# Kernel optimization log

Hardware: AMD Instinct MI355X
Metric: run time of the kernel (lower is better)

The kernel has to match this reference:

```python
import jax, jax.numpy as jnp
import numpy as np

EPS = 1e-5

def _leaky(x):
    return jax.nn.leaky_relu(x, 0.2)

def _bn(x, p, axis):
    # p: [4, C] rows = (gamma, beta, running_mean, running_var); inference-mode BN
    g, b, m, v = p
    scale = g * jax.lax.rsqrt(v + EPS)
    shape = [1] * x.ndim
    shape[axis] = -1
    return x * scale.reshape(shape) + (b - m * scale).reshape(shape)

def _graph_feature(x, k):
    # x: [B, C, N] -> edge features [B, 2C, N, k] (knn on -squared-distance, topk largest)
    B, C, N = x.shape
    xx = jnp.sum(x * x, axis=1)                                   # [B, N]
    pd = 2.0 * jnp.einsum('bcn,bcm->bnm', x, x) - xx[:, :, None] - xx[:, None, :]
    idx = jax.lax.top_k(pd, k)[1]                                 # [B, N, k]
    xt = jnp.transpose(x, (0, 2, 1))                              # [B, N, C]
    nb = xt[jnp.arange(B)[:, None, None], idx]                    # [B, N, k, C]
    ctr = xt[:, :, None, :]
    f = jnp.concatenate([nb - ctr, jnp.broadcast_to(ctr, nb.shape)], axis=-1)
    return jnp.transpose(f, (0, 3, 1, 2))                         # [B, 2C, N, k]

def _cbam(x, fc1, fc2, sw):
    # Channel attention (shared MLP on avg+max pooled) then spatial attention (5x5 conv)
    mlp = lambda v: jax.nn.relu(v @ fc1.T) @ fc2.T
    ca = jax.nn.sigmoid(mlp(jnp.mean(x, (2, 3))) + mlp(jnp.max(x, (2, 3))))
    x = x * ca[:, :, None, None]
    s = jnp.concatenate([jnp.mean(x, 1, keepdims=True), jnp.max(x, 1, keepdims=True)], axis=1)
    sa = jax.lax.conv_general_dilated(s, sw, (1, 1), [(2, 2), (2, 2)],
                                      dimension_numbers=('NCHW', 'OIHW', 'NCHW'))
    return x * jax.nn.sigmoid(sa)

def _edge_block(x, k, W, bn, fc1, fc2, sw):
    f = _graph_feature(x, k)                                      # [B, 2C, N, k]
    f = _leaky(_bn(jnp.einsum('oc,bcnk->bonk', W, f), bn, 1))     # 1x1 conv + BN + LeakyReLU
    f = _cbam(f, fc1, fc2, sw)
    return jnp.max(f, axis=-1)                                    # [B, Cout, N]

def _bn_params(key, c):
    k1, k2, k3, k4 = jax.random.split(key, 4)
    g = 1.0 + 0.1 * jax.random.normal(k1, (c,))
    b = 0.1 * jax.random.normal(k2, (c,))
    m = 0.1 * jax.random.normal(k3, (c,))
    v = 0.5 + jax.random.uniform(k4, (c,))
    return jnp.stack([g, b, m, v])

def setup_inputs() -> dict:
    key = jax.random.key(0)
    nrm = lambda i, shape, s: s * jax.random.normal(jax.random.fold_in(key, i), shape, dtype=jnp.float32)
    d = {}
    d['x'] = jax.random.normal(jax.random.fold_in(key, 0), (4, 3, 2048), dtype=jnp.float32)
    d['W1'] = nrm(1, (64, 6), 0.3)
    d['W2'] = nrm(2, (64, 128), 0.15)
    d['W3'] = nrm(3, (128, 128), 0.15)
    d['W4'] = nrm(4, (256, 256), 0.1)
    d['W5'] = nrm(5, (1024, 512), 0.08)
    for i, c in zip(range(1, 6), [64, 64, 128, 256, 1024]):
        d['bn%d' % i] = _bn_params(jax.random.fold_in(key, 10 + i), c)
    d['bn6'] = _bn_params(jax.random.fold_in(key, 16), 512)
    d['bn7'] = _bn_params(jax.random.fold_in(key, 17), 256)
    for j, c in zip(range(1, 5), [64, 64, 128, 256]):
        r = c // 8
        d['ca%d_fc1' % j] = nrm(20 + j, (r, c), 0.2)
        d['ca%d_fc2' % j] = nrm(30 + j, (c, r), 0.2)
        d['sa%d' % j] = nrm(40 + j, (1, 2, 5, 5), 0.2)
    d['lin1_w'] = nrm(50, (512, 2048), 0.05)
    d['lin2_w'] = nrm(51, (256, 512), 0.08)
    d['lin2_b'] = nrm(52, (256,), 0.05)
    d['lin3_w'] = nrm(53, (40, 256), 0.1)
    d['lin3_b'] = nrm(54, (40,), 0.05)
    d['k'] = 20
    return d

def reference(x, W1, bn1, ca1_fc1, ca1_fc2, sa1, W2, bn2, ca2_fc1, ca2_fc2, sa2,
              W3, bn3, ca3_fc1, ca3_fc2, sa3, W4, bn4, ca4_fc1, ca4_fc2, sa4,
              W5, bn5, lin1_w, bn6, lin2_w, lin2_b, bn7, lin3_w, lin3_b, k):
    x1 = _edge_block(x,  k, W1, bn1, ca1_fc1, ca1_fc2, sa1)   # [B, 64, N]
    x2 = _edge_block(x1, k, W2, bn2, ca2_fc1, ca2_fc2, sa2)   # [B, 64, N]
    x3 = _edge_block(x2, k, W3, bn3, ca3_fc1, ca3_fc2, sa3)   # [B, 128, N]
    x4 = _edge_block(x3, k, W4, bn4, ca4_fc1, ca4_fc2, sa4)   # [B, 256, N]
    xc = jnp.concatenate([x1, x2, x3, x4], axis=1)            # [B, 512, N]
    h = _leaky(_bn(jnp.einsum('oc,bcn->bon', W5, xc), bn5, 1))  # [B, 1024, N]
    g = jnp.concatenate([jnp.max(h, axis=-1), jnp.mean(h, axis=-1)], axis=1)  # [B, 2048]
    g = _leaky(_bn(g @ lin1_w.T, bn6, 1))                     # dropout = identity (eval)
    g = _leaky(_bn(g @ lin2_w.T + lin2_b, bn7, 1))
    return g @ lin3_w.T + lin3_b                              # [B, 40]
```

## Files before the change

kernel.cpp:

```cpp
#include <hip/hip_runtime.h>
#include <math.h>

#define BB 4
#define NN 2048
#define KK 20
#define EPSF 1e-5f
#define TR 4

__device__ __forceinline__ float leaky(float x){ return x > 0.f ? x : 0.2f*x; }
__device__ __forceinline__ float sigm(float x){ return 1.f/(1.f+expf(-x)); }

__global__ void k_xx(const float* __restrict__ X, long bstride, int C, float* __restrict__ xx){
  int i = blockIdx.x*blockDim.x + threadIdx.x;
  int b = i >> 11, n = i & (NN-1);
  const float* xb = X + (long)b*bstride;
  float s = 0.f;
  for (int c = 0; c < C; ++c){ float v = xb[c*NN + n]; s += v*v; }
  xx[i] = s;
}

__global__ __launch_bounds__(256) void k_knn(const float* __restrict__ X, long bstride, int C,
                      const float* __restrict__ xx, int* __restrict__ idx){
  __shared__ unsigned int pdrow[TR][NN];
  int rowsPerB = NN/TR;
  int b = blockIdx.x / rowsPerB;
  int r0 = (blockIdx.x % rowsPerB) * TR;
  const float* xb = X + (long)b*bstride;
  int tid = threadIdx.x;

  float acc[4][8];
  #pragma unroll
  for (int r = 0; r < 4; ++r)
    #pragma unroll
    for (int j = 0; j < 8; ++j) acc[r][j] = 0.f;
  for (int c = 0; c < C; ++c){
    const float* xcp = xb + (long)c*NN;
    float4 ctr = *(const float4*)(xcp + r0);
    float v[8];
    #pragma unroll
    for (int j = 0; j < 8; ++j) v[j] = xcp[tid + 256*j];
    #pragma unroll
    for (int j = 0; j < 8; ++j){
      acc[0][j] = fmaf(ctr.x, v[j], acc[0][j]);
      acc[1][j] = fmaf(ctr.y, v[j], acc[1][j]);
      acc[2][j] = fmaf(ctr.z, v[j], acc[2][j]);
      acc[3][j] = fmaf(ctr.w, v[j], acc[3][j]);
    }
  }
  float xxr[4];
  #pragma unroll
  for (int r = 0; r < 4; ++r) xxr[r] = xx[b*NN + r0 + r];
  #pragma unroll
  for (int j = 0; j < 8; ++j){
    int m = tid + 256*j;
    float xxm = xx[b*NN + m];
    #pragma unroll
    for (int r = 0; r < 4; ++r){
      float pd = 2.f*acc[r][j] - xxr[r] - xxm;
      unsigned u = __float_as_uint(pd);
      u ^= (u & 0x80000000u) ? 0xFFFFFFFFu : 0x80000000u;
      pdrow[r][m] = u;
    }
  }
  __syncthreads();

  int wave = tid >> 6, lane = tid & 63;
  int r = wave;
  unsigned long long k1 = 0ull, k2 = 0ull;
  #pragma unroll
  for (int j = 0; j < 32; ++j){
    int m = lane + (j<<6);
    unsigned long long key = ((unsigned long long)pdrow[r][m] << 11) | (unsigned)(2047 - m);
    if (key > k1){ k2 = k1; k1 = key; }
    else if (key > k2){ k2 = key; }
  }
  unsigned removed = 0u;
  int* orow = idx + ((long)b*NN + r0 + r)*KK;
  for (int sel = 0; sel < KK; ++sel){
    unsigned long long g = k1;
    #pragma unroll
    for (int off = 32; off; off >>= 1){
      unsigned long long o = __shfl_xor(g, off);
      if (o > g) g = o;
    }
    int gm = 2047 - (int)(g & 2047u);
    if (lane == 0) orow[sel] = gm;
    if ((gm & 63) == lane){
      removed |= 1u << (gm >> 6);
      k1 = k2; k2 = 0ull;
      if (k1 == 0ull){
        #pragma unroll
        for (int j = 0; j < 32; ++j){
          if (removed & (1u << j)) continue;
          int m = lane + (j<<6);
          unsigned long long key = ((unsigned long long)pdrow[r][m] << 11) | (unsigned)(2047 - m);
          if (key > k1){ k2 = k1; k1 = key; }
          else if (key > k2){ k2 = key; }
        }
      }
    }
  }
}

__global__ void k_proj(const float* __restrict__ X, long bstride, int C, int Cout,
                       const float* __restrict__ W, const float* __restrict__ bn,
                       float* __restrict__ Pg, float* __restrict__ PgT,
                       float* __restrict__ Pc, float* __restrict__ PcT){
  int nb = NN/256;
  int t = blockIdx.x;
  int nchunk = t % nb; t /= nb;
  int o = t % Cout; int b = t / Cout;
  int m = nchunk*256 + threadIdx.x;
  const float* xb = X + (long)b*bstride;
  float a1 = 0.f, a2 = 0.f;
  for (int c = 0; c < C; ++c){
    float v  = xb[c*NN + m];
    float wl = W[o*2*C + c], wr = W[o*2*C + C + c];
    a1 += wl*v; a2 += (wr - wl)*v;
  }
  float gg = bn[o], bb = bn[Cout+o], mn = bn[2*Cout+o], vv = bn[3*Cout+o];
  float scale = gg * rsqrtf(vv + EPSF);
  float bias  = bb - mn*scale;
  float pg = scale*a1;
  float pc = scale*a2 + bias;
  Pg [((long)b*Cout + o)*NN + m] = pg;
  PgT[((long)b*NN + m)*Cout + o] = pg;
  Pc [((long)b*Cout + o)*NN + m] = pc;
  PcT[((long)b*NN + m)*Cout + o] = pc;
}

__global__ __launch_bounds__(256) void k_proj_t(const float* __restrict__ X, long bstride, int C, int Cout,
                         const float* __restrict__ W, const float* __restrict__ bn,
                         float* __restrict__ Pg, float* __restrict__ PgT,
                         float* __restrict__ Pc, float* __restrict__ PcT){
  __shared__ float xs[32][128];
  __shared__ float wls[64][33];
  __shared__ float wds[64][33];
  int t = blockIdx.x;
  int nb = t & 15; t >>= 4;
  int nob = Cout >> 6;
  int ob = t % nob; int b = t / nob;
  int n0 = nb << 7, o0 = ob << 6;
  int tid = threadIdx.x;
  int tx = tid & 15, ty = tid >> 4;
  const float* xb = X + (long)b*bstride + n0;

  float ag[4][8], ac[4][8];
  #pragma unroll
  for (int i = 0; i < 4; ++i)
    #pragma unroll
    for (int j = 0; j < 8; ++j){ ag[i][j] = 0.f; ac[i][j] = 0.f; }

  for (int cc = 0; cc < C; cc += 32){
    {
      int col4 = tid & 31;
      int ci0 = tid >> 5;
      #pragma unroll
      for (int q = 0; q < 4; ++q){
        int ci = ci0 + (q << 3);
        float4 v = *(const float4*)(xb + (long)(cc + ci)*NN + (col4 << 2));
        *(float4*)&xs[ci][col4 << 2] = v;
      }
    }
    {
      int ci4 = tid & 7;
      int oi0 = tid >> 3;
      #pragma unroll
      for (int q = 0; q < 2; ++q){
        int oi = oi0 + (q << 5);
        const float* wrow = W + (long)(o0 + oi)*2*C + cc + (ci4 << 2);
        float4 wl = *(const float4*)(wrow);
        float4 wr = *(const float4*)(wrow + C);
        wls[oi][(ci4 << 2) + 0] = wl.x;
        wls[oi][(ci4 << 2) + 1] = wl.y;
        wls[oi][(ci4 << 2) + 2] = wl.z;
        wls[oi][(ci4 << 2) + 3] = wl.w;
        wds[oi][(ci4 << 2) + 0] = wr.x - wl.x;
        wds[oi][(ci4 << 2) + 1] = wr.y - wl.y;
        wds[oi][(ci4 << 2) + 2] = wr.z - wl.z;
        wds[oi][(ci4 << 2) + 3] = wr.w - wl.w;
      }
    }
    __syncthreads();
    #pragma unroll 8
    for (int ci = 0; ci < 32; ++ci){
      float4 xa  = *(const float4*)&xs[ci][tx << 2];
      float4 xc2 = *(const float4*)&xs[ci][64 + (tx << 2)];
      #pragma unroll
      for (int oo = 0; oo < 4; ++oo){
        float wl = wls[(ty << 2) + oo][ci];
        float wd = wds[(ty << 2) + oo][ci];
        ag[oo][0] = fmaf(wl, xa.x, ag[oo][0]); ag[oo][1] = fmaf(wl, xa.y, ag[oo][1]);
        ag[oo][2] = fmaf(wl, xa.z, ag[oo][2]); ag[oo][3] = fmaf(wl, xa.w, ag[oo][3]);
        ag[oo][4] = fmaf(wl, xc2.x, ag[oo][4]); ag[oo][5] = fmaf(wl, xc2.y, ag[oo][5]);
        ag[oo][6] = fmaf(wl, xc2.z, ag[oo][6]); ag[oo][7] = fmaf(wl, xc2.w, ag[oo][7]);
        ac[oo][0] = fmaf(wd, xa.x, ac[oo][0]); ac[oo][1] = fmaf(wd, xa.y, ac[oo][1]);
        ac[oo][2] = fmaf(wd, xa.z, ac[oo][2]); ac[oo][3] = fmaf(wd, xa.w, ac[oo][3]);
        ac[oo][4] = fmaf(wd, xc2.x, ac[oo][4]); ac[oo][5] = fmaf(wd, xc2.y, ac[oo][5]);
        ac[oo][6] = fmaf(wd, xc2.z, ac[oo][6]); ac[oo][7] = fmaf(wd, xc2.w, ac[oo][7]);
      }
    }
    __syncthreads();
  }

  float scl[4], bia[4];
  #pragma unroll
  for (int oo = 0; oo < 4; ++oo){
    int o = o0 + (ty << 2) + oo;
    scl[oo] = bn[o] * rsqrtf(bn[3*Cout + o] + EPSF);
    bia[oo] = bn[Cout + o] - bn[2*Cout + o]*scl[oo];
  }
  #pragma unroll
  for (int oo = 0; oo < 4; ++oo){
    long rb = ((long)b*Cout + o0 + (ty << 2) + oo)*NN + n0;
    float4 g0 = {scl[oo]*ag[oo][0], scl[oo]*ag[oo][1], scl[oo]*ag[oo][2], scl[oo]*ag[oo][3]};
    float4 g1 = {scl[oo]*ag[oo][4], scl[oo]*ag[oo][5], scl[oo]*ag[oo][6], scl[oo]*ag[oo][7]};
    float4 c0 = {fmaf(scl[oo], ac[oo][0], bia[oo]), fmaf(scl[oo], ac[oo][1], bia[oo]),
                 fmaf(scl[oo], ac[oo][2], bia[oo]), fmaf(scl[oo], ac[oo][3], bia[oo])};
    float4 c1 = {fmaf(scl[oo], ac[oo][4], bia[oo]), fmaf(scl[oo], ac[oo][5], bia[oo]),
                 fmaf(scl[oo], ac[oo][6], bia[oo]), fmaf(scl[oo], ac[oo][7], bia[oo])};
    *(float4*)(Pg + rb + (tx << 2))      = g0;
    *(float4*)(Pg + rb + 64 + (tx << 2)) = g1;
    *(float4*)(Pc + rb + (tx << 2))      = c0;
    *(float4*)(Pc + rb + 64 + (tx << 2)) = c1;
  }
  #pragma unroll
  for (int j = 0; j < 8; ++j){
    int n = n0 + ((j < 4) ? (tx << 2) + j : 64 + (tx << 2) + (j - 4));
    long rb = ((long)b*NN + n)*Cout + o0 + (ty << 2);
    float4 tg = {scl[0]*ag[0][j], scl[1]*ag[1][j], scl[2]*ag[2][j], scl[3]*ag[3][j]};
    float4 tc = {fmaf(scl[0], ac[0][j], bia[0]), fmaf(scl[1], ac[1][j], bia[1]),
                 fmaf(scl[2], ac[2][j], bia[2]), fmaf(scl[3], ac[3][j], bia[3])};
    *(float4*)(PgT + rb) = tg;
    *(float4*)(PcT + rb) = tc;
  }
}

__global__ void k_cstats(const float* __restrict__ Pg, const float* __restrict__ Pc,
                         const int* __restrict__ idx, int Cout,
                         float* __restrict__ cmean, float* __restrict__ cmax){
  int b = blockIdx.x / Cout, o = blockIdx.x % Cout;
  const float* pg = Pg + ((long)b*Cout + o)*NN;
  const float* pc = Pc + ((long)b*Cout + o)*NN;
  const int* id = idx + (long)b*NN*KK;
  int tid = threadIdx.x;
  float s = 0.f, mx = -INFINITY;
  for (int i = tid; i < NN*KK; i += 256){
    int n = i / KK;
    int iv = id[i];
    float v = leaky(pg[iv] + pc[n]);
    s += v; mx = fmaxf(mx, v);
  }
  __shared__ float ss[256], sm[256];
  ss[tid] = s; sm[tid] = mx; __syncthreads();
  for (int st = 128; st; st >>= 1){
    if (tid < st){ ss[tid] += ss[tid+st]; sm[tid] = fmaxf(sm[tid], sm[tid+st]); }
    __syncthreads();
  }
  if (tid == 0){ cmean[blockIdx.x] = ss[0]/(float)(NN*KK); cmax[blockIdx.x] = sm[0]; }
}

__global__ void k_catt(const float* __restrict__ cmean, const float* __restrict__ cmax,
                       const float* __restrict__ fc1, const float* __restrict__ fc2,
                       int Cout, int r, float* __restrict__ ca){
  int b = blockIdx.x, tid = threadIdx.x;
  __shared__ float h1m[32], h1x[32];
  __shared__ float mv[256], xv[256];
  if (tid < Cout){ mv[tid] = cmean[b*Cout+tid]; xv[tid] = cmax[b*Cout+tid]; }
  __syncthreads();
  if (tid < r){
    float am = 0.f, ax = 0.f;
    for (int c = 0; c < Cout; ++c){ float w = fc1[tid*Cout+c]; am += w*mv[c]; ax += w*xv[c]; }
    h1m[tid] = fmaxf(am, 0.f); h1x[tid] = fmaxf(ax, 0.f);
  }
  __syncthreads();
  if (tid < Cout){
    float a = 0.f;
    for (int j = 0; j < r; ++j) a += fc2[tid*r+j]*(h1m[j] + h1x[j]);
    ca[b*Cout+tid] = sigm(a);
  }
}

__global__ void k_sstats(const float* __restrict__ PgT, const float* __restrict__ PcT,
                         const int* __restrict__ idx, const float* __restrict__ ca,
                         int Cout, float* __restrict__ s){
  long i = (long)blockIdx.x*256 + threadIdx.x;
  int kk = (int)(i % KK); long t = i / KK; int n = (int)(t % NN); int b = (int)(t / NN);
  int iv = idx[((long)b*NN + n)*KK + kk];
  const float4* pg4 = (const float4*)(PgT + ((long)b*NN + iv)*Cout);
  const float4* pc4 = (const float4*)(PcT + ((long)b*NN + n)*Cout);
  const float4* ca4 = (const float4*)(ca + b*Cout);
  float sum = 0.f, mx = -INFINITY;
  int q = Cout >> 2;
  for (int o = 0; o < q; ++o){
    float4 a = pg4[o], c = pc4[o], w = ca4[o];
    float v0 = leaky(a.x + c.x) * w.x;
    float v1 = leaky(a.y + c.y) * w.y;
    float v2 = leaky(a.z + c.z) * w.z;
    float v3 = leaky(a.w + c.w) * w.w;
    sum += v0; mx = fmaxf(mx, v0);
    sum += v1; mx = fmaxf(mx, v1);
    sum += v2; mx = fmaxf(mx, v2);
    sum += v3; mx = fmaxf(mx, v3);
  }
  s[((long)b*2*NN + n)*KK + kk]      = sum/(float)Cout;
  s[((long)b*2*NN + NN + n)*KK + kk] = mx;
}

__global__ void k_sconv(const float* __restrict__ s, const float* __restrict__ sw,
                        float* __restrict__ sa){
  long i = (long)blockIdx.x*256 + threadIdx.x;
  int kk = (int)(i % KK); long t = i / KK; int n = (int)(t % NN); int b = (int)(t / NN);
  float acc = 0.f;
  for (int ci = 0; ci < 2; ++ci)
    for (int dy = 0; dy < 5; ++dy){
      int nn = n + dy - 2; if (nn < 0 || nn >= NN) continue;
      for (int dx = 0; dx < 5; ++dx){
        int kx = kk + dx - 2; if (kx < 0 || kx >= KK) continue;
        acc += sw[ci*25 + dy*5 + dx] * s[((long)b*2*NN + ci*NN + nn)*KK + kx];
      }
    }
  sa[i] = sigm(acc);
}

__global__ void k_final(const float* __restrict__ Pg, const float* __restrict__ Pc,
                        const int* __restrict__ idx, const float* __restrict__ ca,
                        const float* __restrict__ sa, int Cout, int outoff,
                        float* __restrict__ xc){
  long i = (long)blockIdx.x*256 + threadIdx.x;
  int n = (int)(i % NN); long t = i / NN; int o = (int)(t % Cout); int b = (int)(t / Cout);
  const float* pg = Pg + ((long)b*Cout + o)*NN;
  float pcv = Pc[((long)b*Cout + o)*NN + n];
  float cav = ca[b*Cout + o];
  const int* id   = idx + ((long)b*NN + n)*KK;
  const float* sb = sa  + ((long)b*NN + n)*KK;
  float mx = -INFINITY;
  for (int kk = 0; kk < KK; ++kk){
    float v = leaky(pg[id[kk]] + pcv) * cav * sb[kk];
    mx = fmaxf(mx, v);
  }
  xc[((long)b*512 + outoff + o)*NN + n] = mx;
}

__global__ __launch_bounds__(256) void k_gemm5(const float* __restrict__ xc, const float* __restrict__ W5,
                        const float* __restrict__ bn5, float* __restrict__ gpart){
  __shared__ float xs[32][128];
  __shared__ float wsd[64][33];
  int t = blockIdx.x;
  int nb = t & 15; t >>= 4;
  int ob = t & 15; int b = t >> 4;
  int n0 = nb << 7, o0 = ob << 6;
  int tid = threadIdx.x;
  int tx = tid & 15, ty = tid >> 4;
  const float* xb = xc + (long)b*512*NN + n0;

  float acc[4][8];
  #pragma unroll
  for (int i = 0; i < 4; ++i)
    #pragma unroll
    for (int j = 0; j < 8; ++j) acc[i][j] = 0.f;

  for (int cc = 0; cc < 16; ++cc){
    {
      int col4 = tid & 31;
      int ci0 = tid >> 5;
      #pragma unroll
      for (int q = 0; q < 4; ++q){
        int ci = ci0 + (q << 3);
        float4 v = *(const float4*)(xb + (long)(cc*32 + ci)*NN + (col4 << 2));
        *(float4*)&xs[ci][col4 << 2] = v;
      }
    }
    {
      int ci4 = tid & 7;
      int oi0 = tid >> 3;
      #pragma unroll
      for (int q = 0; q < 2; ++q){
        int oi = oi0 + (q << 5);
        float4 w = *(const float4*)(W5 + (long)(o0 + oi)*512 + cc*32 + (ci4 << 2));
        wsd[oi][(ci4 << 2) + 0] = w.x;
        wsd[oi][(ci4 << 2) + 1] = w.y;
        wsd[oi][(ci4 << 2) + 2] = w.z;
        wsd[oi][(ci4 << 2) + 3] = w.w;
      }
    }
    __syncthreads();
    #pragma unroll 8
    for (int ci = 0; ci < 32; ++ci){
      float4 xa = *(const float4*)&xs[ci][tx << 2];
      float4 xc2 = *(const float4*)&xs[ci][64 + (tx << 2)];
      float w0 = wsd[(ty << 2) + 0][ci];
      float w1 = wsd[(ty << 2) + 1][ci];
      float w2 = wsd[(ty << 2) + 2][ci];
      float w3 = wsd[(ty << 2) + 3][ci];
      acc[0][0] = fmaf(w0, xa.x, acc[0][0]); acc[0][1] = fmaf(w0, xa.y, acc[0][1]);
      acc[0][2] = fmaf(w0, xa.z, acc[0][2]); acc[0][3] = fmaf(w0, xa.w, acc[0][3]);
      acc[0][4] = fmaf(w0, xc2.x, acc[0][4]); acc[0][5] = fmaf(w0, xc2.y, acc[0][5]);
      acc[0][6] = fmaf(w0, xc2.z, acc[0][6]); acc[0][7] = fmaf(w0, xc2.w, acc[0][7]);
      acc[1][0] = fmaf(w1, xa.x, acc[1][0]); acc[1][1] = fmaf(w1, xa.y, acc[1][1]);
      acc[1][2] = fmaf(w1, xa.z, acc[1][2]); acc[1][3] = fmaf(w1, xa.w, acc[1][3]);
      acc[1][4] = fmaf(w1, xc2.x, acc[1][4]); acc[1][5] = fmaf(w1, xc2.y, acc[1][5]);
      acc[1][6] = fmaf(w1, xc2.z, acc[1][6]); acc[1][7] = fmaf(w1, xc2.w, acc[1][7]);
      acc[2][0] = fmaf(w2, xa.x, acc[2][0]); acc[2][1] = fmaf(w2, xa.y, acc[2][1]);
      acc[2][2] = fmaf(w2, xa.z, acc[2][2]); acc[2][3] = fmaf(w2, xa.w, acc[2][3]);
      acc[2][4] = fmaf(w2, xc2.x, acc[2][4]); acc[2][5] = fmaf(w2, xc2.y, acc[2][5]);
      acc[2][6] = fmaf(w2, xc2.z, acc[2][6]); acc[2][7] = fmaf(w2, xc2.w, acc[2][7]);
      acc[3][0] = fmaf(w3, xa.x, acc[3][0]); acc[3][1] = fmaf(w3, xa.y, acc[3][1]);
      acc[3][2] = fmaf(w3, xa.z, acc[3][2]); acc[3][3] = fmaf(w3, xa.w, acc[3][3]);
      acc[3][4] = fmaf(w3, xc2.x, acc[3][4]); acc[3][5] = fmaf(w3, xc2.y, acc[3][5]);
      acc[3][6] = fmaf(w3, xc2.z, acc[3][6]); acc[3][7] = fmaf(w3, xc2.w, acc[3][7]);
    }
    __syncthreads();
  }

  float psum[4], pmax[4];
  #pragma unroll
  for (int oo = 0; oo < 4; ++oo){
    int o = o0 + (ty << 2) + oo;
    float scale = bn5[o] * rsqrtf(bn5[3072 + o] + EPSF);
    float bias  = bn5[1024 + o] - bn5[2048 + o] * scale;
    float s = 0.f, mx = -INFINITY;
    #pragma unroll
    for (int j = 0; j < 8; ++j){
      float v = leaky(fmaf(scale, acc[oo][j], bias));
      s += v; mx = fmaxf(mx, v);
    }
    psum[oo] = s; pmax[oo] = mx;
  }
  __syncthreads();
  float* ps = &xs[0][0];
  float* pm = ps + 64*17;
  #pragma unroll
  for (int oo = 0; oo < 4; ++oo){
    int o = (ty << 2) + oo;
    ps[o*17 + tx] = psum[oo];
    pm[o*17 + tx] = pmax[oo];
  }
  __syncthreads();
  if (tid < 64){
    float s = 0.f, mx = -INFINITY;
    #pragma unroll
    for (int j = 0; j < 16; ++j){
      s += ps[tid*17 + j];
      mx = fmaxf(mx, pm[tid*17 + j]);
    }
    long base = ((long)(b*16 + nb))*1024 + o0 + tid;
    gpart[base] = s;
    gpart[65536 + base] = mx;
  }
}

__global__ void k_pool2(const float* __restrict__ gpart, float* __restrict__ g){
  int i = blockIdx.x*256 + threadIdx.x;
  int b = i >> 10, o = i & 1023;
  float s = 0.f, mx = -INFINITY;
  for (int nb = 0; nb < 16; ++nb){
    s += gpart[((long)(b*16 + nb))*1024 + o];
    mx = fmaxf(mx, gpart[65536 + ((long)(b*16 + nb))*1024 + o]);
  }
  g[b*2048 + o] = mx;
  g[b*2048 + 1024 + o] = s * (1.f/2048.f);
}

__global__ void k_dense(const float* __restrict__ in, const float* __restrict__ w,
                        const float* __restrict__ bias, const float* __restrict__ bnp,
                        int Cin, int Cout, float* __restrict__ out){
  int b = blockIdx.x / Cout, j = blockIdx.x % Cout;
  int tid = threadIdx.x;
  float a = 0.f;
  for (int c = tid; c < Cin; c += 256) a += w[(long)j*Cin + c]*in[(long)b*Cin + c];
  __shared__ float ss[256];
  ss[tid] = a; __syncthreads();
  for (int st = 128; st; st >>= 1){
    if (tid < st) ss[tid] += ss[tid+st];
    __syncthreads();
  }
  if (tid == 0){
    float v = ss[0];
    if (bias) v += bias[j];
    if (bnp){
      float scale = bnp[j]*rsqrtf(bnp[3*Cout+j] + EPSF);
      float bb    = bnp[Cout+j] - bnp[2*Cout+j]*scale;
      v = leaky(v*scale + bb);
    }
    out[b*Cout + j] = v;
  }
}

extern "C" void kernel_launch(void* const* d_in, const int* in_sizes, int n_in,
                              void* d_out, int out_size, void* d_ws, size_t ws_size,
                              hipStream_t stream){
  (void)in_sizes; (void)n_in; (void)out_size;
  const float* x  = (const float*)d_in[0];
  const float* Wb[4]  = {(const float*)d_in[1], (const float*)d_in[2], (const float*)d_in[3], (const float*)d_in[4]};
  const float* W5     = (const float*)d_in[5];
  const float* bnb[4] = {(const float*)d_in[6], (const float*)d_in[7], (const float*)d_in[8], (const float*)d_in[9]};
  const float* bn5    = (const float*)d_in[10];
  const float* bn6    = (const float*)d_in[11];
  const float* bn7    = (const float*)d_in[12];
  const float* fc1b[4] = {(const float*)d_in[13], (const float*)d_in[16], (const float*)d_in[19], (const float*)d_in[22]};
  const float* fc2b[4] = {(const float*)d_in[14], (const float*)d_in[17], (const float*)d_in[20], (const float*)d_in[23]};
  const float* swb[4]  = {(const float*)d_in[15], (const float*)d_in[18], (const float*)d_in[21], (const float*)d_in[24]};
  const float* lin1_w = (const float*)d_in[25];
  const float* lin2_w = (const float*)d_in[26];
  const float* lin2_b = (const float*)d_in[27];
  const float* lin3_w = (const float*)d_in[28];
  const float* lin3_b = (const float*)d_in[29];

  float* ws = (float*)d_ws;
  float* xc = ws;
  float* tb = ws + (size_t)BB*512*NN;
  float* xx   = tb;
  int*   idx  = (int*)(tb + 8192);
  float* Pg   = tb + 8192 + 163840;
  float* PgT  = Pg  + 2097152;
  float* Pc   = PgT + 2097152;
  float* PcT  = Pc  + 2097152;
  float* cmean = PcT + 2097152;
  float* cmax  = cmean + 1024;
  float* ca    = cmax + 1024;
  float* s     = ca + 1024;
  float* sa    = s + 327680;
  float* gpart = tb;
  float* g  = tb + 131072;
  float* t1 = g + 8192;
  float* t2 = t1 + 2048;
  size_t needed = ((size_t)BB*512*NN + 9055232) * 4;
  if (ws_size < needed) return;

  const int Cin [4] = {3, 64, 64, 128};
  const int Cout[4] = {64, 64, 128, 256};
  const int inoff[4]  = {0, 0, 64, 128};
  const int outoff[4] = {0, 64, 128, 256};

  for (int blk = 0; blk < 4; ++blk){
    const float* Xp; long bstr;
    if (blk == 0){ Xp = x; bstr = 3l*NN; }
    else { Xp = xc + (long)inoff[blk]*NN; bstr = 512l*NN; }
    int C = Cin[blk], Co = Cout[blk];
    hipLaunchKernelGGL(k_xx,    dim3(BB*NN/256), dim3(256), 0, stream, Xp, bstr, C, xx);
    hipLaunchKernelGGL(k_knn,   dim3(BB*NN/TR),  dim3(256), 0, stream, Xp, bstr, C, xx, idx);
    if (blk == 0){
      hipLaunchKernelGGL(k_proj,  dim3(BB*Co*(NN/256)), dim3(256), 0, stream, Xp, bstr, C, Co, Wb[blk], bnb[blk], Pg, PgT, Pc, PcT);
    } else {
      hipLaunchKernelGGL(k_proj_t, dim3(BB*(Co>>6)*16), dim3(256), 0, stream, Xp, bstr, C, Co, Wb[blk], bnb[blk], Pg, PgT, Pc, PcT);
    }
    hipLaunchKernelGGL(k_cstats, dim3(BB*Co), dim3(256), 0, stream, Pg, Pc, idx, Co, cmean, cmax);
    hipLaunchKernelGGL(k_catt,  dim3(BB), dim3(256), 0, stream, cmean, cmax, fc1b[blk], fc2b[blk], Co, Co/8, ca);
    hipLaunchKernelGGL(k_sstats, dim3(BB*NN*KK/256), dim3(256), 0, stream, PgT, PcT, idx, ca, Co, s);
    hipLaunchKernelGGL(k_sconv, dim3(BB*NN*KK/256), dim3(256), 0, stream, s, swb[blk], sa);
    hipLaunchKernelGGL(k_final, dim3(BB*Co*NN/256), dim3(256), 0, stream, Pg, Pc, idx, ca, sa, Co, outoff[blk], xc);
  }
  hipLaunchKernelGGL(k_gemm5, dim3(BB*16*16), dim3(256), 0, stream, xc, W5, bn5, gpart);
  hipLaunchKernelGGL(k_pool2, dim3(16), dim3(256), 0, stream, gpart, g);
  hipLaunchKernelGGL(k_dense, dim3(BB*512), dim3(256), 0, stream, g,  lin1_w, (const float*)nullptr, bn6, 2048, 512, t1);
  hipLaunchKernelGGL(k_dense, dim3(BB*256), dim3(256), 0, stream, t1, lin2_w, lin2_b, bn7, 512, 256, t2);
  hipLaunchKernelGGL(k_dense, dim3(BB*40),  dim3(256), 0, stream, t2, lin3_w, lin3_b, (const float*)nullptr, 256, 40, (float*)d_out);
}
```

Measured before the change: 1.110 ms.

## Restructure kNN kernel: 8 rows per block, chunked distances, bitonic-sorted top-k

The kNN kernel now handles 8 query rows per block, processing the 2048 candidates in two chunks of 1024 with float4 loads and an 8x4 register tile per thread, which halves shared memory and improves reuse of the loaded candidate columns. Each lane keeps a top-4 per row, and the per-lane heads are bitonic-sorted across the wave, so every selection reads lane 0 and inserts the owner's next candidate through a ballot instead of a full shuffle-max reduction. When a lane exhausts its top-4, it recomputes distances from global memory because the chunked shared buffer no longer holds the whole row. That fallback is slow and divergent, but it should rarely run.

```diff
diff --git a/kernel.cpp b/kernel.cpp
--- a/kernel.cpp
+++ b/kernel.cpp
@@ -5,10 +5,30 @@
 #define NN 2048
 #define KK 20
 #define EPSF 1e-5f
-#define TR 4
 
 __device__ __forceinline__ float leaky(float x){ return x > 0.f ? x : 0.2f*x; }
 __device__ __forceinline__ float sigm(float x){ return 1.f/(1.f+expf(-x)); }
+
+__device__ __forceinline__ unsigned long long shfl64(unsigned long long v, int src){
+  int lo = __shfl((int)(unsigned)(v & 0xffffffffull), src, 64);
+  int hi = __shfl((int)(unsigned)(v >> 32), src, 64);
+  return ((unsigned long long)(unsigned)hi << 32) | (unsigned)lo;
+}
+__device__ __forceinline__ unsigned long long shflxor64(unsigned long long v, int m){
+  int lo = __shfl_xor((int)(unsigned)(v & 0xffffffffull), m, 64);
+  int hi = __shfl_xor((int)(unsigned)(v >> 32), m, 64);
+  return ((unsigned long long)(unsigned)hi << 32) | (unsigned)lo;
+}
+__device__ __forceinline__ unsigned long long shfldn64(unsigned long long v){
+  int lo = __shfl_down((int)(unsigned)(v & 0xffffffffull), 1, 64);
+  int hi = __shfl_down((int)(unsigned)(v >> 32), 1, 64);
+  return ((unsigned long long)(unsigned)hi << 32) | (unsigned)lo;
+}
+__device__ __forceinline__ void ce64(unsigned long long &a, unsigned long long &b){
+  unsigned long long mx = a > b ? a : b;
+  unsigned long long mn = a > b ? b : a;
+  a = mx; b = mn;
+}
 
 __global__ void k_xx(const float* __restrict__ X, long bstride, int C, float* __restrict__ xx){
   int i = blockIdx.x*blockDim.x + threadIdx.x;
@@ -21,83 +41,130 @@
 
 __global__ __launch_bounds__(256) void k_knn(const float* __restrict__ X, long bstride, int C,
                       const float* __restrict__ xx, int* __restrict__ idx){
-  __shared__ unsigned int pdrow[TR][NN];
-  int rowsPerB = NN/TR;
-  int b = blockIdx.x / rowsPerB;
-  int r0 = (blockIdx.x % rowsPerB) * TR;
+  __shared__ unsigned int pdc[8][1024];
+  int b = blockIdx.x >> 8;
+  int r0 = (blockIdx.x & 255) << 3;
   const float* xb = X + (long)b*bstride;
+  const float* xxb = xx + b*NN;
   int tid = threadIdx.x;
-
-  float acc[4][8];
-  #pragma unroll
-  for (int r = 0; r < 4; ++r)
-    #pragma unroll
-    for (int j = 0; j < 8; ++j) acc[r][j] = 0.f;
-  for (int c = 0; c < C; ++c){
-    const float* xcp = xb + (long)c*NN;
-    float4 ctr = *(const float4*)(xcp + r0);
-    float v[8];
-    #pragma unroll
-    for (int j = 0; j < 8; ++j) v[j] = xcp[tid + 256*j];
-    #pragma unroll
-    for (int j = 0; j < 8; ++j){
-      acc[0][j] = fmaf(ctr.x, v[j], acc[0][j]);
-      acc[1][j] = fmaf(ctr.y, v[j], acc[1][j]);
-      acc[2][j] = fmaf(ctr.z, v[j], acc[2][j]);
-      acc[3][j] = fmaf(ctr.w, v[j], acc[3][j]);
-    }
-  }
-  float xxr[4];
-  #pragma unroll
-  for (int r = 0; r < 4; ++r) xxr[r] = xx[b*NN + r0 + r];
-  #pragma unroll
-  for (int j = 0; j < 8; ++j){
-    int m = tid + 256*j;
-    float xxm = xx[b*NN + m];
-    #pragma unroll
-    for (int r = 0; r < 4; ++r){
-      float pd = 2.f*acc[r][j] - xxr[r] - xxm;
-      unsigned u = __float_as_uint(pd);
-      u ^= (u & 0x80000000u) ? 0xFFFFFFFFu : 0x80000000u;
-      pdrow[r][m] = u;
-    }
-  }
-  __syncthreads();
-
-  int wave = tid >> 6, lane = tid & 63;
-  int r = wave;
-  unsigned long long k1 = 0ull, k2 = 0ull;
-  #pragma unroll
-  for (int j = 0; j < 32; ++j){
-    int m = lane + (j<<6);
-    unsigned long long key = ((unsigned long long)pdrow[r][m] << 11) | (unsigned)(2047 - m);
-    if (key > k1){ k2 = k1; k1 = key; }
-    else if (key > k2){ k2 = key; }
-  }
-  unsigned removed = 0u;
-  int* orow = idx + ((long)b*NN + r0 + r)*KK;
-  for (int sel = 0; sel < KK; ++sel){
-    unsigned long long g = k1;
-    #pragma unroll
-    for (int off = 32; off; off >>= 1){
-      unsigned long long o = __shfl_xor(g, off);
-      if (o > g) g = o;
-    }
-    int gm = 2047 - (int)(g & 2047u);
-    if (lane == 0) orow[sel] = gm;
-    if ((gm & 63) == lane){
-      removed |= 1u << (gm >> 6);
-      k1 = k2; k2 = 0ull;
-      if (k1 == 0ull){
-        #pragma unroll
-        for (int j = 0; j < 32; ++j){
-          if (removed & (1u << j)) continue;
-          int m = lane + (j<<6);
-          unsigned long long key = ((unsigned long long)pdrow[r][m] << 11) | (unsigned)(2047 - m);
-          if (key > k1){ k2 = k1; k1 = key; }
-          else if (key > k2){ k2 = key; }
+  int lane = tid & 63, wave = tid >> 6;
+
+  float4 xra = *(const float4*)(xxb + r0);
+  float4 xrb = *(const float4*)(xxb + r0 + 4);
+  float xs8[8] = {xra.x,xra.y,xra.z,xra.w,xrb.x,xrb.y,xrb.z,xrb.w};
+
+  unsigned long long L[2][4];
+  #pragma unroll
+  for (int rp = 0; rp < 2; ++rp)
+    #pragma unroll
+    for (int q = 0; q < 4; ++q) L[rp][q] = 0ull;
+
+  for (int ch = 0; ch < 2; ++ch){
+    int m0 = (ch << 10) + (tid << 2);
+    float acc[8][4];
+    #pragma unroll
+    for (int r = 0; r < 8; ++r){ acc[r][0]=0.f; acc[r][1]=0.f; acc[r][2]=0.f; acc[r][3]=0.f; }
+    for (int c = 0; c < C; ++c){
+      const float* xcp = xb + (long)c*NN;
+      float4 ca = *(const float4*)(xcp + r0);
+      float4 cb = *(const float4*)(xcp + r0 + 4);
+      float4 v  = *(const float4*)(xcp + m0);
+      float cr[8] = {ca.x,ca.y,ca.z,ca.w,cb.x,cb.y,cb.z,cb.w};
+      #pragma unroll
+      for (int r = 0; r < 8; ++r){
+        acc[r][0]=fmaf(cr[r],v.x,acc[r][0]);
+        acc[r][1]=fmaf(cr[r],v.y,acc[r][1]);
+        acc[r][2]=fmaf(cr[r],v.z,acc[r][2]);
+        acc[r][3]=fmaf(cr[r],v.w,acc[r][3]);
+      }
+    }
+    float4 xmv = *(const float4*)(xxb + m0);
+    float xm4[4] = {xmv.x,xmv.y,xmv.z,xmv.w};
+    #pragma unroll
+    for (int r = 0; r < 8; ++r){
+      unsigned u[4];
+      #pragma unroll
+      for (int q = 0; q < 4; ++q){
+        float pd = 2.f*acc[r][q] - xs8[r] - xm4[q];
+        unsigned uu = __float_as_uint(pd);
+        uu ^= (uu & 0x80000000u) ? 0xFFFFFFFFu : 0x80000000u;
+        u[q] = uu;
+      }
+      *(uint4*)&pdc[r][tid << 2] = make_uint4(u[0],u[1],u[2],u[3]);
+    }
+    __syncthreads();
+    #pragma unroll
+    for (int rp = 0; rp < 2; ++rp){
+      int row = (wave << 1) + rp;
+      #pragma unroll
+      for (int jj = 0; jj < 16; ++jj){
+        int mloc = lane + (jj << 6);
+        int m = (ch << 10) + mloc;
+        unsigned long long key = ((unsigned long long)pdc[row][mloc] << 11) | (unsigned)(2047 - m);
+        L[rp][3] = L[rp][3] > key ? L[rp][3] : key;
+        ce64(L[rp][2], L[rp][3]);
+        ce64(L[rp][1], L[rp][2]);
+        ce64(L[rp][0], L[rp][1]);
+      }
+    }
+    __syncthreads();
+  }
+
+  #pragma unroll
+  for (int rp = 0; rp < 2; ++rp){
+    int rowg = r0 + (wave << 1) + rp;
+    int* orow = idx + ((long)b*NN + rowg)*KK;
+    float xxrow = xxb[rowg];
+    unsigned removed = 0u;
+    unsigned long long S = L[rp][0], sp0 = L[rp][1], sp1 = L[rp][2], sp2 = L[rp][3];
+    #pragma unroll
+    for (int k = 2; k <= 64; k <<= 1){
+      #pragma unroll
+      for (int d = k >> 1; d > 0; d >>= 1){
+        unsigned long long o = shflxor64(S, d);
+        bool takeMax = ((lane & k) == 0) == ((lane & d) == 0);
+        unsigned long long mx = S > o ? S : o;
+        unsigned long long mn = S > o ? o : S;
+        S = takeMax ? mx : mn;
+      }
+    }
+    for (int sel = 0; sel < KK; ++sel){
+      unsigned long long g = shfl64(S, 0);
+      int gm = 2047 - (int)(g & 2047ull);
+      if (lane == 0) orow[sel] = gm;
+      if (sel == KK-1) break;
+      int owner = gm & 63;
+      unsigned long long r = 0ull;
+      bool need = false;
+      if (lane == owner){
+        removed |= 1u << (gm >> 6);
+        r = sp0; sp0 = sp1; sp1 = sp2; sp2 = 0ull;
+        need = (r == 0ull);
+      }
+      if (__any((int)need)){
+        if (need){
+          unsigned long long a0=0ull,a1=0ull,a2=0ull,a3=0ull;
+          for (int j = 0; j < 32; ++j){
+            if ((removed >> j) & 1u) continue;
+            int m = lane + (j << 6);
+            float d = 0.f;
+            for (int c = 0; c < C; ++c)
+              d = fmaf(xb[(long)c*NN + rowg], xb[(long)c*NN + m], d);
+            float pd = 2.f*d - xxrow - xxb[m];
+            unsigned uu = __float_as_uint(pd);
+            uu ^= (uu & 0x80000000u) ? 0xFFFFFFFFu : 0x80000000u;
+            unsigned long long key = ((unsigned long long)uu << 11) | (unsigned)(2047 - m);
+            a3 = a3 > key ? a3 : key;
+            ce64(a2,a3); ce64(a1,a2); ce64(a0,a1);
+          }
+          r = a0; sp0 = a1; sp1 = a2; sp2 = a3;
         }
       }
+      unsigned long long T = shfldn64(S);
+      unsigned long long rb = shfl64(r, owner);
+      unsigned long long bal = __ballot(S > rb);
+      int q = (int)__builtin_popcountll(bal) - 1;
+      S = (lane < q) ? T : (lane == q ? rb : S);
     }
   }
 }
@@ -539,7 +606,7 @@
     else { Xp = xc + (long)inoff[blk]*NN; bstr = 512l*NN; }
     int C = Cin[blk], Co = Cout[blk];
     hipLaunchKernelGGL(k_xx,    dim3(BB*NN/256), dim3(256), 0, stream, Xp, bstr, C, xx);
-    hipLaunchKernelGGL(k_knn,   dim3(BB*NN/TR),  dim3(256), 0, stream, Xp, bstr, C, xx, idx);
+    hipLaunchKernelGGL(k_knn,   dim3(BB*NN/8),   dim3(256), 0, stream, Xp, bstr, C, xx, idx);
     if (blk == 0){
       hipLaunchKernelGGL(k_proj,  dim3(BB*Co*(NN/256)), dim3(256), 0, stream, Xp, bstr, C, Co, Wb[blk], bnb[blk], Pg, PgT, Pc, PcT);
     } else {
```

Measured after the change: 1.985 ms. 78.8% more time.
